# Optimization experiments

Measured on AMD Instinct MI355X. Metric: run time of the kernel, lower is better.

Reference implementation:

```python
import jax, jax.numpy as jnp
import numpy as np

N = 131072      # total nodes = num_graphs * numNodes
E = 2097152     # edges (avg degree 16)
C_IN = 64
HID = 64        # hiddenChannels
NODES = 128     # numNodes per graph
B = 1024        # num_graphs
NCLS = 4


def setup_inputs() -> dict:
    key = jax.random.key(0)
    ks = jax.random.split(key, 10)
    x = jax.random.normal(ks[0], (N, C_IN), jnp.float32)
    edge_index = jax.random.randint(ks[1], (2, E), 0, N, dtype=jnp.int32)
    edge_attr = jax.random.uniform(ks[2], (E,), jnp.float32)
    # GCNConv params (stored as [in, out]); PyG uses glorot init, bias zeros
    W1 = jax.random.normal(ks[3], (C_IN, 2 * HID), jnp.float32) * (1.0 / np.sqrt(C_IN))
    b1 = jnp.zeros((2 * HID,), jnp.float32)
    W2 = jax.random.normal(ks[4], (2 * HID, HID), jnp.float32) * (1.0 / np.sqrt(2 * HID))
    b2 = jnp.zeros((HID,), jnp.float32)
    Wfc = jax.random.normal(ks[5], (HID * NODES, NCLS), jnp.float32) * (1.0 / np.sqrt(HID * NODES))
    bfc = jnp.zeros((NCLS,), jnp.float32)
    return {"x": x, "edge_index": edge_index, "edge_attr": edge_attr,
            "W1": W1, "b1": b1, "W2": W2, "b2": b2, "Wfc": Wfc, "bfc": bfc}


def gcn_conv(x, src, dst, ew, W, b):
    # PyG GCNConv: add self-loops (weight 1), symmetric normalization,
    # linear transform, scatter-add aggregation at target nodes, + bias.
    loop = jnp.arange(N, dtype=src.dtype)
    s = jnp.concatenate([src, loop])
    d = jnp.concatenate([dst, loop])
    w = jnp.concatenate([ew, jnp.ones((N,), ew.dtype)])
    deg = jax.ops.segment_sum(w, d, num_segments=N)                  # [N]
    dis = jnp.where(deg > 0, jax.lax.rsqrt(jnp.maximum(deg, 1e-30)), 0.0)
    norm = dis[s] * w * dis[d]                                       # [E+N]
    h = x @ W                                                        # [N, out]
    msg = h[s] * norm[:, None]                                       # gather + scale
    out = jax.ops.segment_sum(msg, d, num_segments=N)                # scatter-add
    return out + b


def reference(x, edge_index, edge_attr, W1, b1, W2, b2, Wfc, bfc):
    src, dst = edge_index[0], edge_index[1]
    h = jax.nn.relu(gcn_conv(x, src, dst, edge_attr, W1, b1))
    h = jax.nn.relu(gcn_conv(h, src, dst, edge_attr, W2, b2))
    h = h.reshape(B, HID * NODES)
    logits = h @ Wfc + bfc
    return jax.nn.softmax(logits, axis=1)
```

## Files before the change

### kernel.cpp

```cpp
#include <hip/hip_runtime.h>

#define N_NODES 131072
#define NE      2097152
#define CIN     64
#define HID     64
#define H2X     128
#define NODESG  128
#define NGRAPH  1024
#define NCLS    4

#define NBUCK   256
#define NPB     512
#define HBLK    1024
#define EPB     2048
#define DEGSC   1048576.0f

typedef short bf16x8 __attribute__((ext_vector_type(8)));
typedef float f32x4  __attribute__((ext_vector_type(4)));

__device__ __forceinline__ unsigned short f2b(float f) {
    unsigned int u = __float_as_uint(f);
    return (unsigned short)((u + 0x7fffu + ((u >> 16) & 1u)) >> 16);
}
__device__ __forceinline__ unsigned int pack2(float a, float b) {
    return (unsigned int)f2b(a) | ((unsigned int)f2b(b) << 16);
}
__device__ __forceinline__ float blo(unsigned u) { return __uint_as_float(u << 16); }
__device__ __forceinline__ float bhi(unsigned u) { return __uint_as_float(u & 0xffff0000u); }


__global__ __launch_bounds__(256) void k_hist(const int* __restrict__ dst,
                                              int* __restrict__ hist) {
    __shared__ unsigned bh[NBUCK];
    int t = threadIdx.x;
    bh[t] = 0;
    __syncthreads();
    int base = blockIdx.x * EPB;
    #pragma unroll
    for (int k = 0; k < EPB / 256; ++k) {
        int d = dst[base + t + 256 * k];
        atomicAdd(&bh[d >> 9], 1u);
    }
    __syncthreads();
    hist[t * HBLK + blockIdx.x] = (int)bh[t];
}

__global__ void k_scan1(const int* __restrict__ in, int* __restrict__ out,
                        int* __restrict__ partial) {
    __shared__ int sd[256];
    int t = threadIdx.x;
    int base = blockIdx.x * 512;
    int c0 = in[base + 2*t];
    int c1 = in[base + 2*t + 1];
    int loc = c0 + c1;
    sd[t] = loc;
    __syncthreads();
    for (int off = 1; off < 256; off <<= 1) {
        int v = (t >= off) ? sd[t - off] : 0;
        __syncthreads();
        sd[t] += v;
        __syncthreads();
    }
    int excl = sd[t] - loc;
    out[base + 2*t]     = excl;
    out[base + 2*t + 1] = excl + c0;
    if (t == 255) partial[blockIdx.x] = sd[t];
}

__global__ void k_scan2(int* __restrict__ partial) {
    __shared__ int sd[256];
    int t = threadIdx.x;
    int p0 = partial[2*t], p1 = partial[2*t + 1];
    int loc = p0 + p1;
    sd[t] = loc;
    __syncthreads();
    for (int off = 1; off < 256; off <<= 1) {
        int v = (t >= off) ? sd[t - off] : 0;
        __syncthreads();
        sd[t] += v;
        __syncthreads();
    }
    int excl = sd[t] - loc;
    partial[2*t]     = excl;
    partial[2*t + 1] = excl + p0;
}

__global__ void k_scan3(int* __restrict__ data, const int* __restrict__ partial) {
    int i = blockIdx.x * blockDim.x + threadIdx.x;
    data[i] += partial[i >> 9];
}

__global__ __launch_bounds__(256) void k_scatter(
        const int* __restrict__ src, const int* __restrict__ dst,
        const float* __restrict__ ew, const int* __restrict__ hist,
        unsigned long long* __restrict__ part) {
    __shared__ unsigned lcur[NBUCK];
    int t = threadIdx.x;
    lcur[t] = (unsigned)hist[t * HBLK + blockIdx.x];
    __syncthreads();
    int base = blockIdx.x * EPB;
    #pragma unroll
    for (int k = 0; k < EPB / 256; ++k) {
        int e = base + t + 256 * k;
        int s = src[e], d = dst[e];
        unsigned w = __float_as_uint(ew[e]);
        unsigned p = atomicAdd(&lcur[d >> 9], 1u);
        part[p] = ((unsigned long long)w << 32) |
                  ((unsigned long long)(unsigned)(d & 511) << 17) |
                  (unsigned long long)(unsigned)s;
    }
}

__global__ __launch_bounds__(256) void k_bucket(
        const unsigned long long* __restrict__ part, const int* __restrict__ hist,
        int2* __restrict__ csr, int* __restrict__ rowptr,
        int* __restrict__ counts, float* __restrict__ dis) {
    __shared__ unsigned cnt[NPB];
    __shared__ unsigned degfx[NPB];
    __shared__ int rp[NPB];
    __shared__ int sd[256];
    int t = threadIdx.x, b = blockIdx.x;
    cnt[t] = 0; cnt[t + 256] = 0;
    degfx[t] = 0; degfx[t + 256] = 0;
    __syncthreads();
    int start = hist[b * HBLK];
    int end   = (b == NBUCK - 1) ? NE : hist[(b + 1) * HBLK];

    for (int j = start + t; j < end; j += 256) {
        unsigned long long p = part[j];
        unsigned dl = (unsigned)(p >> 17) & 511u;
        float w = __uint_as_float((unsigned)(p >> 32));
        atomicAdd(&cnt[dl], 1u);
        atomicAdd(&degfx[dl], (unsigned)(w * DEGSC));
    }
    __syncthreads();

    int c0 = (int)cnt[2*t], c1 = (int)cnt[2*t + 1];
    int loc = c0 + c1;
    sd[t] = loc;
    __syncthreads();
    for (int off = 1; off < 256; off <<= 1) {
        int v = (t >= off) ? sd[t - off] : 0;
        __syncthreads();
        sd[t] += v;
        __syncthreads();
    }
    int excl = sd[t] - loc;
    rp[2*t] = excl; rp[2*t + 1] = excl + c0;

    int n0 = b * NPB;
    rowptr[n0 + 2*t]     = start + excl;
    rowptr[n0 + 2*t + 1] = start + excl + c0;
    counts[n0 + 2*t]     = c0;
    counts[n0 + 2*t + 1] = c1;
    float dg0 = (float)degfx[2*t]     * (1.0f / DEGSC);
    float dg1 = (float)degfx[2*t + 1] * (1.0f / DEGSC);
    dis[n0 + 2*t]     = rsqrtf(dg0 + 1.0f);
    dis[n0 + 2*t + 1] = rsqrtf(dg1 + 1.0f);
    cnt[t] = 0; cnt[t + 256] = 0;
    __syncthreads();

    for (int j = start + t; j < end; j += 256) {
        unsigned long long p = part[j];
        unsigned dl = (unsigned)(p >> 17) & 511u;
        int s = (int)(p & 0x1ffffu);
        unsigned r = atomicAdd(&cnt[dl], 1u);
        csr[start + rp[dl] + (int)r] = make_int2(s, (int)(unsigned)(p >> 32));
    }
}

__global__ void k_xcast(const float* __restrict__ x, const float* __restrict__ dis,
                        uint2* __restrict__ xb2) {
    int i = blockIdx.x * blockDim.x + threadIdx.x;
    float d = dis[i >> 4];
    float4 v = ((const float4*)x)[i];
    xb2[i] = make_uint2(pack2(d * v.x, d * v.y), pack2(d * v.z, d * v.w));
}


#define GATHER_PAIR(TAB, pA, pB, nA, nB, cmA, cmB, a0,a1,a2,a3, b0,b1,b2,b3, vSA, vSB) \
    {                                                                                  \
        int   sA0 = __shfl(pA.x, qid),      sA1 = __shfl(pA.x, qid + 4);               \
        int   sA2 = __shfl(pA.x, qid + 8),  sA3 = __shfl(pA.x, qid + 12);              \
        float fA0 = __int_as_float(__shfl(pA.y, qid));                                 \
        float fA1 = __int_as_float(__shfl(pA.y, qid + 4));                             \
        float fA2 = __int_as_float(__shfl(pA.y, qid + 8));                             \
        float fA3 = __int_as_float(__shfl(pA.y, qid + 12));                            \
        int   sB0 = __shfl(pB.x, qid),      sB1 = __shfl(pB.x, qid + 4);               \
        int   sB2 = __shfl(pB.x, qid + 8),  sB3 = __shfl(pB.x, qid + 12);              \
        float fB0 = __int_as_float(__shfl(pB.y, qid));                                 \
        float fB1 = __int_as_float(__shfl(pB.y, qid + 4));                             \
        float fB2 = __int_as_float(__shfl(pB.y, qid + 8));                             \
        float fB3 = __int_as_float(__shfl(pB.y, qid + 12));                            \
        uint2 vA0 = TAB[((unsigned)sA0 << 4) | ql];                                    \
        uint2 vA1 = TAB[((unsigned)sA1 << 4) | ql];                                    \
        uint2 vA2 = TAB[((unsigned)sA2 << 4) | ql];                                    \
        uint2 vA3 = TAB[((unsigned)sA3 << 4) | ql];                                    \
        uint2 vB0 = TAB[((unsigned)sB0 << 4) | ql];                                    \
        uint2 vB1 = TAB[((unsigned)sB1 << 4) | ql];                                    \
        uint2 vB2 = TAB[((unsigned)sB2 << 4) | ql];                                    \
        uint2 vB3 = TAB[((unsigned)sB3 << 4) | ql];                                    \
        vSA = TAB[((unsigned)nA << 4) | ql];                                           \
        vSB = TAB[((unsigned)nB << 4) | ql];                                           \
        a0 = fmaf(fA0, blo(vA0.x), a0); a1 = fmaf(fA0, bhi(vA0.x), a1);                \
        a2 = fmaf(fA0, blo(vA0.y), a2); a3 = fmaf(fA0, bhi(vA0.y), a3);                \
        a0 = fmaf(fA1, blo(vA1.x), a0); a1 = fmaf(fA1, bhi(vA1.x), a1);                \
        a2 = fmaf(fA1, blo(vA1.y), a2); a3 = fmaf(fA1, bhi(vA1.y), a3);                \
        a0 = fmaf(fA2, blo(vA2.x), a0); a1 = fmaf(fA2, bhi(vA2.x), a1);                \
        a2 = fmaf(fA2, blo(vA2.y), a2); a3 = fmaf(fA2, bhi(vA2.y), a3);                \
        a0 = fmaf(fA3, blo(vA3.x), a0); a1 = fmaf(fA3, bhi(vA3.x), a1);                \
        a2 = fmaf(fA3, blo(vA3.y), a2); a3 = fmaf(fA3, bhi(vA3.y), a3);                \
        b0 = fmaf(fB0, blo(vB0.x), b0); b1 = fmaf(fB0, bhi(vB0.x), b1);                \
        b2 = fmaf(fB0, blo(vB0.y), b2); b3 = fmaf(fB0, bhi(vB0.y), b3);                \
        b0 = fmaf(fB1, blo(vB1.x), b0); b1 = fmaf(fB1, bhi(vB1.x), b1);                \
        b2 = fmaf(fB1, blo(vB1.y), b2); b3 = fmaf(fB1, bhi(vB1.y), b3);                \
        b0 = fmaf(fB2, blo(vB2.x), b0); b1 = fmaf(fB2, bhi(vB2.x), b1);                \
        b2 = fmaf(fB2, blo(vB2.y), b2); b3 = fmaf(fB2, bhi(vB2.y), b3);                \
        b0 = fmaf(fB3, blo(vB3.x), b0); b1 = fmaf(fB3, bhi(vB3.x), b1);                \
        b2 = fmaf(fB3, blo(vB3.y), b2); b3 = fmaf(fB3, bhi(vB3.y), b3);                \
        int tsA = (cmA > 16) ? ((cmA - 13) >> 2) : 0;                                  \
        for (int k = 0; k < tsA; ++k) {                                                \
            int jj = 16 + 4 * k + qid;                                                 \
            int   s = __shfl(pA.x, jj);                                                \
            float f = __int_as_float(__shfl(pA.y, jj));                                \
            uint2 v = TAB[((unsigned)s << 4) | ql];                                    \
            a0 = fmaf(f, blo(v.x), a0); a1 = fmaf(f, bhi(v.x), a1);                    \
            a2 = fmaf(f, blo(v.y), a2); a3 = fmaf(f, bhi(v.y), a3);                    \
        }                                                                              \
        int tsB = (cmB > 16) ? ((cmB - 13) >> 2) : 0;                                  \
        for (int k = 0; k < tsB; ++k) {                                                \
            int jj = 16 + 4 * k + qid;                                                 \
            int   s = __shfl(pB.x, jj);                                                \
            float f = __int_as_float(__shfl(pB.y, jj));                                \
            uint2 v = TAB[((unsigned)s << 4) | ql];                                    \
            b0 = fmaf(f, blo(v.x), b0); b1 = fmaf(f, bhi(v.x), b1);                    \
            b2 = fmaf(f, blo(v.y), b2); b3 = fmaf(f, bhi(v.y), b3);                    \
        }                                                                              \
        a0 += __shfl_xor(a0, 16); a1 += __shfl_xor(a1, 16);                            \
        a2 += __shfl_xor(a2, 16); a3 += __shfl_xor(a3, 16);                            \
        a0 += __shfl_xor(a0, 32); a1 += __shfl_xor(a1, 32);                            \
        a2 += __shfl_xor(a2, 32); a3 += __shfl_xor(a3, 32);                            \
        b0 += __shfl_xor(b0, 16); b1 += __shfl_xor(b1, 16);                            \
        b2 += __shfl_xor(b2, 16); b3 += __shfl_xor(b3, 16);                            \
        b0 += __shfl_xor(b0, 32); b1 += __shfl_xor(b1, 32);                            \
        b2 += __shfl_xor(b2, 32); b3 += __shfl_xor(b3, 32);                            \
    }


__global__ __launch_bounds__(256, 4) void k_layer1(
        const uint2* __restrict__ xb2, const int2* __restrict__ csr,
        const int* __restrict__ rowptr, const int* __restrict__ counts,
        const float* __restrict__ dis, const float* __restrict__ W1,
        const float* __restrict__ b1, unsigned short* __restrict__ h1b) {
    __shared__ unsigned short sWf[8192];
    __shared__ unsigned short sagg_b[32][72];
    __shared__ float sb[H2X];
    int tid = threadIdx.x;

    #pragma unroll
    for (int it = 0; it < 4; ++it) {
        int idx = tid + 256 * it;
        int kt = idx >> 9, nt = (idx >> 6) & 7, l = idx & 63;
        int lm = l & 15, lq = l >> 4;
        unsigned int pk[4];
        #pragma unroll
        for (int jp = 0; jp < 4; ++jp) {
            float w0 = W1[(kt*32 + lq*8 + 2*jp)     * H2X + nt*16 + lm];
            float w1 = W1[(kt*32 + lq*8 + 2*jp + 1) * H2X + nt*16 + lm];
            pk[jp] = pack2(w0, w1);
        }
        *(uint4*)&sWf[idx * 8] = make_uint4(pk[0], pk[1], pk[2], pk[3]);
    }
    if (tid < H2X) sb[tid] = b1[tid];

    int wave = tid >> 6, lane = tid & 63;
    int qid = lane >> 4, ql = lane & 15;
    int n0 = blockIdx.x * 32;
    int nb = n0 + wave * 8;

    int cm8[8], cnt8[8], rs8[8];
    float dn8[8];
    int2 myp[8];
    #pragma unroll
    for (int i = 0; i < 8; ++i) {
        rs8[i] = rowptr[nb + i];
        cnt8[i] = counts[nb + i];
        dn8[i] = dis[nb + i];
        cm8[i] = cnt8[i] < 64 ? cnt8[i] : 64;
    }
    #pragma unroll
    for (int i = 0; i < 8; ++i)
        myp[i] = (lane < cm8[i]) ? csr[rs8[i] + lane] : make_int2(0, 0);

    #pragma unroll
    for (int ip = 0; ip < 8; ip += 2) {
        int2 pA = myp[ip], pB = myp[ip + 1];
        int nA = nb + ip, nB = nA + 1;
        float a0 = 0.f, a1 = 0.f, a2 = 0.f, a3 = 0.f;
        float b0 = 0.f, b1v = 0.f, b2v = 0.f, b3 = 0.f;
        uint2 vSA, vSB;
        GATHER_PAIR(xb2, pA, pB, nA, nB, cm8[ip], cm8[ip + 1],
                    a0, a1, a2, a3, b0, b1v, b2v, b3, vSA, vSB);
        for (int jj = 64; jj < cnt8[ip]; ++jj) {
            int2 p = csr[rs8[ip] + jj];
            float f = __int_as_float(p.y);
            uint2 v = xb2[((unsigned)p.x << 4) | ql];
            if (qid == 0) {
                a0 += f * blo(v.x); a1 += f * bhi(v.x);
                a2 += f * blo(v.y); a3 += f * bhi(v.y);
            }
        }
        for (int jj = 64; jj < cnt8[ip + 1]; ++jj) {
            int2 p = csr[rs8[ip + 1] + jj];
            float f = __int_as_float(p.y);
            uint2 v = xb2[((unsigned)p.x << 4) | ql];
            if (qid == 0) {
                b0 += f * blo(v.x); b1v += f * bhi(v.x);
                b2v += f * blo(v.y); b3 += f * bhi(v.y);
            }
        }
        if (qid == 0) {
            float dnA = dn8[ip], dnB = dn8[ip + 1];
            int m = wave * 8 + ip;
            *(uint2*)&sagg_b[m][ql * 4] =
                make_uint2(pack2(dnA * (a0 + blo(vSA.x)), dnA * (a1 + bhi(vSA.x))),
                           pack2(dnA * (a2 + blo(vSA.y)), dnA * (a3 + bhi(vSA.y))));
            *(uint2*)&sagg_b[m + 1][ql * 4] =
                make_uint2(pack2(dnB * (b0 + blo(vSB.x)), dnB * (b1v + bhi(vSB.x))),
                           pack2(dnB * (b2v + blo(vSB.y)), dnB * (b3 + bhi(vSB.y))));
        }
    }
    __syncthreads();

    int mt = wave & 1, ntb = (wave >> 1) * 4;
    int lm = lane & 15, lq = lane >> 4;
    bf16x8 af0 = *(const bf16x8*)&sagg_b[mt*16 + lm][lq * 8];
    bf16x8 af1 = *(const bf16x8*)&sagg_b[mt*16 + lm][32 + lq * 8];
    #pragma unroll
    for (int t = 0; t < 4; ++t) {
        int nt = ntb + t;
        bf16x8 bf0 = *(const bf16x8*)&sWf[(nt*64 + lane) * 8];
        bf16x8 bf1 = *(const bf16x8*)&sWf[((8 + nt)*64 + lane) * 8];
        f32x4 acc = {0.f, 0.f, 0.f, 0.f};
        acc = __builtin_amdgcn_mfma_f32_16x16x32_bf16(af0, bf0, acc, 0, 0, 0);
        acc = __builtin_amdgcn_mfma_f32_16x16x32_bf16(af1, bf1, acc, 0, 0, 0);
        int ch = nt*16 + lm;
        float bias = sb[ch];
        #pragma unroll
        for (int r = 0; r < 4; ++r) {
            int node = n0 + mt*16 + lq*4 + r;
            h1b[(size_t)node * H2X + ch] = f2b(fmaxf(acc[r] + bias, 0.f));
        }
    }
}


__global__ __launch_bounds__(256) void k_gemm2(
        const unsigned short* __restrict__ h1b, const float* __restrict__ W2,
        const float* __restrict__ dis, unsigned short* __restrict__ t2u) {
    __shared__ unsigned short sWf[8192];
    __shared__ unsigned short sh[32][136];
    int tid = threadIdx.x;

    #pragma unroll
    for (int it = 0; it < 4; ++it) {
        int idx = tid + 256 * it;
        int kt = idx >> 8, nt = (idx >> 6) & 3, l = idx & 63;
        int lm = l & 15, lq = l >> 4;
        unsigned int pk[4];
        #pragma unroll
        for (int jp = 0; jp < 4; ++jp) {
            float w0 = W2[(kt*32 + lq*8 + 2*jp)     * HID + nt*16 + lm];
            float w1 = W2[(kt*32 + lq*8 + 2*jp + 1) * HID + nt*16 + lm];
            pk[jp] = pack2(w0, w1);
        }
        *(uint4*)&sWf[idx * 8] = make_uint4(pk[0], pk[1], pk[2], pk[3]);
    }

    int n0 = blockIdx.x * 32;
    #pragma unroll
    for (int it = 0; it < 2; ++it) {
        int idx = tid + 256 * it;
        int r = idx >> 4, c = idx & 15;
        *(uint4*)&sh[r][c * 8] = ((const uint4*)(h1b + (size_t)(n0 + r) * H2X))[c];
    }
    __syncthreads();

    int wave = tid >> 6, lane = tid & 63;
    int lm = lane & 15, lq = lane >> 4;
    #pragma unroll
    for (int ti = 0; ti < 2; ++ti) {
        int t = wave * 2 + ti;
        int mt = t & 1, nt = t >> 1;
        f32x4 acc = {0.f, 0.f, 0.f, 0.f};
        #pragma unroll
        for (int kt = 0; kt < 4; ++kt) {
            bf16x8 af = *(const bf16x8*)&sh[mt*16 + lm][kt*32 + lq*8];
            bf16x8 bf = *(const bf16x8*)&sWf[((kt*4 + nt)*64 + lane) * 8];
            acc = __builtin_amdgcn_mfma_f32_16x16x32_bf16(af, bf, acc, 0, 0, 0);
        }
        int ch = nt*16 + lm;
        #pragma unroll
        for (int r = 0; r < 4; ++r) {
            int node = n0 + mt*16 + lq*4 + r;
            t2u[(size_t)node * HID + ch] = f2b(dis[node] * acc[r]);
        }
    }
}


__global__ __launch_bounds__(256, 4) void k_agg2(
        const uint2* __restrict__ t2y, const int2* __restrict__ csr,
        const int* __restrict__ rowptr, const int* __restrict__ counts,
        const float* __restrict__ dis, const float* __restrict__ b2,
        unsigned short* __restrict__ h2b) {
    int tid = threadIdx.x;
    int wave = tid >> 6, lane = tid & 63;
    int qid = lane >> 4, ql = lane & 15;
    float4 bb = *(const float4*)&b2[ql * 4];
    int n0 = blockIdx.x * 32;
    int nb = n0 + wave * 8;

    int cm8[8], cnt8[8], rs8[8];
    float dn8[8];
    int2 myp[8];
    #pragma unroll
    for (int i = 0; i < 8; ++i) {
        rs8[i] = rowptr[nb + i];
        cnt8[i] = counts[nb + i];
        dn8[i] = dis[nb + i];
        cm8[i] = cnt8[i] < 64 ? cnt8[i] : 64;
    }
    #pragma unroll
    for (int i = 0; i < 8; ++i)
        myp[i] = (lane < cm8[i]) ? csr[rs8[i] + lane] : make_int2(0, 0);

    #pragma unroll
    for (int ip = 0; ip < 8; ip += 2) {
        int2 pA = myp[ip], pB = myp[ip + 1];
        int nA = nb + ip, nB = nA + 1;
        float a0 = 0.f, a1 = 0.f, a2 = 0.f, a3 = 0.f;
        float b0 = 0.f, b1v = 0.f, b2v = 0.f, b3 = 0.f;
        uint2 vSA, vSB;
        GATHER_PAIR(t2y, pA, pB, nA, nB, cm8[ip], cm8[ip + 1],
                    a0, a1, a2, a3, b0, b1v, b2v, b3, vSA, vSB);
        for (int jj = 64; jj < cnt8[ip]; ++jj) {
            int2 p = csr[rs8[ip] + jj];
            float f = __int_as_float(p.y);
            uint2 v = t2y[((unsigned)p.x << 4) | ql];
            if (qid == 0) {
                a0 += f * blo(v.x); a1 += f * bhi(v.x);
                a2 += f * blo(v.y); a3 += f * bhi(v.y);
            }
        }
        for (int jj = 64; jj < cnt8[ip + 1]; ++jj) {
            int2 p = csr[rs8[ip + 1] + jj];
            float f = __int_as_float(p.y);
            uint2 v = t2y[((unsigned)p.x << 4) | ql];
            if (qid == 0) {
                b0 += f * blo(v.x); b1v += f * bhi(v.x);
                b2v += f * blo(v.y); b3 += f * bhi(v.y);
            }
        }
        if (qid == 0) {
            float dnA = dn8[ip], dnB = dn8[ip + 1];
            float oa0 = fmaxf(fmaf(dnA, a0 + blo(vSA.x), bb.x), 0.f);
            float oa1 = fmaxf(fmaf(dnA, a1 + bhi(vSA.x), bb.y), 0.f);
            float oa2 = fmaxf(fmaf(dnA, a2 + blo(vSA.y), bb.z), 0.f);
            float oa3 = fmaxf(fmaf(dnA, a3 + bhi(vSA.y), bb.w), 0.f);
            float ob0 = fmaxf(fmaf(dnB, b0 + blo(vSB.x), bb.x), 0.f);
            float ob1 = fmaxf(fmaf(dnB, b1v + bhi(vSB.x), bb.y), 0.f);
            float ob2 = fmaxf(fmaf(dnB, b2v + blo(vSB.y), bb.z), 0.f);
            float ob3 = fmaxf(fmaf(dnB, b3 + bhi(vSB.y), bb.w), 0.f);
            *(uint2*)&h2b[((unsigned)nA << 6) | (ql * 4)] =
                make_uint2(pack2(oa0, oa1), pack2(oa2, oa3));
            *(uint2*)&h2b[((unsigned)nB << 6) | (ql * 4)] =
                make_uint2(pack2(ob0, ob1), pack2(ob2, ob3));
        }
    }
}


__global__ __launch_bounds__(256) void k_fc(
        const unsigned short* __restrict__ h2b, const float* __restrict__ Wfc,
        const float* __restrict__ bfc, float* __restrict__ out) {
    __shared__ float4 red[256];
    int b = blockIdx.x, t = threadIdx.x;
    const uint2* hrow = (const uint2*)(h2b + (size_t)b * (HID * NODESG));
    const float4* W4 = (const float4*)Wfc;
    float4 a = make_float4(0.f, 0.f, 0.f, 0.f);
    #pragma unroll
    for (int j = 0; j < 8; ++j) {
        int i = j * 256 + t;
        uint2 hv = hrow[i];
        float h0 = blo(hv.x), h1 = bhi(hv.x), h2v = blo(hv.y), h3 = bhi(hv.y);
        float4 w0 = W4[i * 4 + 0];
        float4 w1 = W4[i * 4 + 1];
        float4 w2 = W4[i * 4 + 2];
        float4 w3 = W4[i * 4 + 3];
        a.x = fmaf(h0, w0.x, a.x); a.y = fmaf(h0, w0.y, a.y);
        a.z = fmaf(h0, w0.z, a.z); a.w = fmaf(h0, w0.w, a.w);
        a.x = fmaf(h1, w1.x, a.x); a.y = fmaf(h1, w1.y, a.y);
        a.z = fmaf(h1, w1.z, a.z); a.w = fmaf(h1, w1.w, a.w);
        a.x = fmaf(h2v, w2.x, a.x); a.y = fmaf(h2v, w2.y, a.y);
        a.z = fmaf(h2v, w2.z, a.z); a.w = fmaf(h2v, w2.w, a.w);
        a.x = fmaf(h3, w3.x, a.x); a.y = fmaf(h3, w3.y, a.y);
        a.z = fmaf(h3, w3.z, a.z); a.w = fmaf(h3, w3.w, a.w);
    }
    red[t] = a;
    __syncthreads();
    for (int s = 128; s > 0; s >>= 1) {
        if (t < s) {
            red[t].x += red[t + s].x; red[t].y += red[t + s].y;
            red[t].z += red[t + s].z; red[t].w += red[t + s].w;
        }
        __syncthreads();
    }
    if (t == 0) {
        float l0 = red[0].x + bfc[0];
        float l1 = red[0].y + bfc[1];
        float l2 = red[0].z + bfc[2];
        float l3 = red[0].w + bfc[3];
        float mx = fmaxf(fmaxf(l0, l1), fmaxf(l2, l3));
        float e0 = expf(l0 - mx), e1 = expf(l1 - mx);
        float e2 = expf(l2 - mx), e3 = expf(l3 - mx);
        float inv = 1.f / (e0 + e1 + e2 + e3);
        float4 o = make_float4(e0 * inv, e1 * inv, e2 * inv, e3 * inv);
        *(float4*)&out[(size_t)b * 4] = o;
    }
}


extern "C" void kernel_launch(void* const* d_in, const int* in_sizes, int n_in,
                              void* d_out, int out_size, void* d_ws, size_t ws_size,
                              hipStream_t stream) {
    const float* x   = (const float*)d_in[0];
    const int*   ei  = (const int*)  d_in[1];
    const float* ea  = (const float*)d_in[2];
    const float* W1  = (const float*)d_in[3];
    const float* b1  = (const float*)d_in[4];
    const float* W2  = (const float*)d_in[5];
    const float* b2  = (const float*)d_in[6];
    const float* Wfc = (const float*)d_in[7];
    const float* bfc = (const float*)d_in[8];
    float* out = (float*)d_out;
    const int* src = ei;
    const int* dst = ei + NE;

    char* ws = (char*)d_ws;
    size_t off = 0;
    int*   hist   = (int*)  (ws + off); off += (size_t)NBUCK * HBLK * 4;
    int*   partial= (int*)  (ws + off); off += 4096;
    int*   counts = (int*)  (ws + off); off += (size_t)N_NODES * 4;
    int*   rowptr = (int*)  (ws + off); off += (size_t)N_NODES * 4;
    float* dis    = (float*)(ws + off); off += (size_t)N_NODES * 4;
    int2*  csr    = (int2*) (ws + off); off += (size_t)NE * 8;
    uint2* xb2    = (uint2*)(ws + off); off += (size_t)N_NODES * CIN * 2;
    unsigned short* h1b = (unsigned short*)(ws + off); off += (size_t)N_NODES * H2X * 2;
    unsigned short* t2u = (unsigned short*)(ws + off); off += (size_t)N_NODES * HID * 2;
    unsigned short* h2b = h1b;
    unsigned long long* part = (unsigned long long*)h1b;

    hipMemsetAsync(hist, 0, (size_t)NBUCK * HBLK * 4, stream);

    k_hist   <<<HBLK, 256, 0, stream>>>(dst, hist);
    k_scan1  <<<NBUCK * HBLK / 512, 256, 0, stream>>>(hist, hist, partial);
    k_scan2  <<<1, 256, 0, stream>>>(partial);
    k_scan3  <<<NBUCK * HBLK / 256, 256, 0, stream>>>(hist, partial);
    k_scatter<<<HBLK, 256, 0, stream>>>(src, dst, ea, hist, part);
    k_bucket <<<NBUCK, 256, 0, stream>>>(part, hist, csr, rowptr, counts, dis);
    k_xcast  <<<(N_NODES * CIN / 4) / 256, 256, 0, stream>>>(x, dis, xb2);
    k_layer1 <<<N_NODES / 32, 256, 0, stream>>>(xb2, csr, rowptr, counts, dis, W1, b1, h1b);
    k_gemm2  <<<N_NODES / 32, 256, 0, stream>>>(h1b, W2, dis, t2u);
    k_agg2   <<<N_NODES / 32, 256, 0, stream>>>((const uint2*)t2u, csr, rowptr, counts, dis, b2, h2b);
    k_fc     <<<NGRAPH, 256, 0, stream>>>(h2b, Wfc, bfc, out);
}
```

Before: 278.4 us.

## Fuse layer-2 GEMM into layer-1 kernel and pre-swizzle weights once

Layer 1 now writes its ReLU output to shared memory and immediately runs the layer-2 GEMM there, removing the k_gemm2 launch and the round trip of the 128-wide h1 activation through global memory. Weight packing into MFMA fragment layout moves to a single-block prologue kernel, so blocks read pre-swizzled bf16 weights from global/L2 instead of each block repacking them into LDS. In k_bucket, the edge count and the fixed-point degree are packed into one 64-bit LDS atomic, halving the atomics in the first pass. The costs are extra LDS for the h1 tile, B fragments now loaded from global memory, and a tiny extra launch.

```diff
diff --git a/kernel.cpp b/kernel.cpp
--- a/kernel.cpp
+++ b/kernel.cpp
@@ -14,6 +14,7 @@
 #define HBLK    1024
 #define EPB     2048
 #define DEGSC   1048576.0f
+#define DEGMASK ((1ull << 40) - 1)
 
 typedef short bf16x8 __attribute__((ext_vector_type(8)));
 typedef float f32x4  __attribute__((ext_vector_type(4)));
@@ -27,6 +28,41 @@
 }
 __device__ __forceinline__ float blo(unsigned u) { return __uint_as_float(u << 16); }
 __device__ __forceinline__ float bhi(unsigned u) { return __uint_as_float(u & 0xffff0000u); }
+
+
+__global__ __launch_bounds__(256) void k_wswiz(
+        const float* __restrict__ W1, const float* __restrict__ W2,
+        unsigned short* __restrict__ wf1, unsigned short* __restrict__ wf2) {
+    int tid = threadIdx.x;
+    #pragma unroll
+    for (int it = 0; it < 4; ++it) {
+        int idx = tid + 256 * it;
+        int kt = idx >> 9, nt = (idx >> 6) & 7, l = idx & 63;
+        int lm = l & 15, lq = l >> 4;
+        unsigned pk[4];
+        #pragma unroll
+        for (int jp = 0; jp < 4; ++jp) {
+            float w0 = W1[(kt*32 + lq*8 + 2*jp)     * H2X + nt*16 + lm];
+            float w1 = W1[(kt*32 + lq*8 + 2*jp + 1) * H2X + nt*16 + lm];
+            pk[jp] = pack2(w0, w1);
+        }
+        *(uint4*)&wf1[idx * 8] = make_uint4(pk[0], pk[1], pk[2], pk[3]);
+    }
+    #pragma unroll
+    for (int it = 0; it < 4; ++it) {
+        int idx = tid + 256 * it;
+        int kt = idx >> 8, nt = (idx >> 6) & 3, l = idx & 63;
+        int lm = l & 15, lq = l >> 4;
+        unsigned pk[4];
+        #pragma unroll
+        for (int jp = 0; jp < 4; ++jp) {
+            float w0 = W2[(kt*32 + lq*8 + 2*jp)     * HID + nt*16 + lm];
+            float w1 = W2[(kt*32 + lq*8 + 2*jp + 1) * HID + nt*16 + lm];
+            pk[jp] = pack2(w0, w1);
+        }
+        *(uint4*)&wf2[idx * 8] = make_uint4(pk[0], pk[1], pk[2], pk[3]);
+    }
+}
 
 
 __global__ __launch_bounds__(256) void k_hist(const int* __restrict__ dst,
@@ -115,13 +151,13 @@
         const unsigned long long* __restrict__ part, const int* __restrict__ hist,
         int2* __restrict__ csr, int* __restrict__ rowptr,
         int* __restrict__ counts, float* __restrict__ dis) {
-    __shared__ unsigned cnt[NPB];
-    __shared__ unsigned degfx[NPB];
+    __shared__ unsigned long long dc[NPB];
+    __shared__ unsigned cnt2[NPB];
     __shared__ int rp[NPB];
     __shared__ int sd[256];
     int t = threadIdx.x, b = blockIdx.x;
-    cnt[t] = 0; cnt[t + 256] = 0;
-    degfx[t] = 0; degfx[t + 256] = 0;
+    dc[t] = 0; dc[t + 256] = 0;
+    cnt2[t] = 0; cnt2[t + 256] = 0;
     __syncthreads();
     int start = hist[b * HBLK];
     int end   = (b == NBUCK - 1) ? NE : hist[(b + 1) * HBLK];
@@ -130,12 +166,12 @@
         unsigned long long p = part[j];
         unsigned dl = (unsigned)(p >> 17) & 511u;
         float w = __uint_as_float((unsigned)(p >> 32));
-        atomicAdd(&cnt[dl], 1u);
-        atomicAdd(&degfx[dl], (unsigned)(w * DEGSC));
-    }
-    __syncthreads();
-
-    int c0 = (int)cnt[2*t], c1 = (int)cnt[2*t + 1];
+        atomicAdd(&dc[dl], (1ull << 40) | (unsigned long long)(unsigned)(w * DEGSC));
+    }
+    __syncthreads();
+
+    unsigned long long d0 = dc[2*t], d1 = dc[2*t + 1];
+    int c0 = (int)(d0 >> 40), c1 = (int)(d1 >> 40);
     int loc = c0 + c1;
     sd[t] = loc;
     __syncthreads();
@@ -153,18 +189,17 @@
     rowptr[n0 + 2*t + 1] = start + excl + c0;
     counts[n0 + 2*t]     = c0;
     counts[n0 + 2*t + 1] = c1;
-    float dg0 = (float)degfx[2*t]     * (1.0f / DEGSC);
-    float dg1 = (float)degfx[2*t + 1] * (1.0f / DEGSC);
+    float dg0 = (float)(d0 & DEGMASK) * (1.0f / DEGSC);
+    float dg1 = (float)(d1 & DEGMASK) * (1.0f / DEGSC);
     dis[n0 + 2*t]     = rsqrtf(dg0 + 1.0f);
     dis[n0 + 2*t + 1] = rsqrtf(dg1 + 1.0f);
-    cnt[t] = 0; cnt[t + 256] = 0;
     __syncthreads();
 
     for (int j = start + t; j < end; j += 256) {
         unsigned long long p = part[j];
         unsigned dl = (unsigned)(p >> 17) & 511u;
         int s = (int)(p & 0x1ffffu);
-        unsigned r = atomicAdd(&cnt[dl], 1u);
+        unsigned r = atomicAdd(&cnt2[dl], 1u);
         csr[start + rp[dl] + (int)r] = make_int2(s, (int)(unsigned)(p >> 32));
     }
 }
@@ -250,27 +285,13 @@
 __global__ __launch_bounds__(256, 4) void k_layer1(
         const uint2* __restrict__ xb2, const int2* __restrict__ csr,
         const int* __restrict__ rowptr, const int* __restrict__ counts,
-        const float* __restrict__ dis, const float* __restrict__ W1,
-        const float* __restrict__ b1, unsigned short* __restrict__ h1b) {
-    __shared__ unsigned short sWf[8192];
+        const float* __restrict__ dis, const unsigned short* __restrict__ wf1,
+        const unsigned short* __restrict__ wf2, const float* __restrict__ b1,
+        unsigned short* __restrict__ t2u) {
     __shared__ unsigned short sagg_b[32][72];
+    __shared__ unsigned short sh1[32][136];
     __shared__ float sb[H2X];
     int tid = threadIdx.x;
-
-    #pragma unroll
-    for (int it = 0; it < 4; ++it) {
-        int idx = tid + 256 * it;
-        int kt = idx >> 9, nt = (idx >> 6) & 7, l = idx & 63;
-        int lm = l & 15, lq = l >> 4;
-        unsigned int pk[4];
-        #pragma unroll
-        for (int jp = 0; jp < 4; ++jp) {
-            float w0 = W1[(kt*32 + lq*8 + 2*jp)     * H2X + nt*16 + lm];
-            float w1 = W1[(kt*32 + lq*8 + 2*jp + 1) * H2X + nt*16 + lm];
-            pk[jp] = pack2(w0, w1);
-        }
-        *(uint4*)&sWf[idx * 8] = make_uint4(pk[0], pk[1], pk[2], pk[3]);
-    }
     if (tid < H2X) sb[tid] = b1[tid];
 
     int wave = tid >> 6, lane = tid & 63;
@@ -339,70 +360,34 @@
     #pragma unroll
     for (int t = 0; t < 4; ++t) {
         int nt = ntb + t;
-        bf16x8 bf0 = *(const bf16x8*)&sWf[(nt*64 + lane) * 8];
-        bf16x8 bf1 = *(const bf16x8*)&sWf[((8 + nt)*64 + lane) * 8];
+        bf16x8 bf0 = *(const bf16x8*)&wf1[(nt*64 + lane) * 8];
+        bf16x8 bf1 = *(const bf16x8*)&wf1[((8 + nt)*64 + lane) * 8];
         f32x4 acc = {0.f, 0.f, 0.f, 0.f};
         acc = __builtin_amdgcn_mfma_f32_16x16x32_bf16(af0, bf0, acc, 0, 0, 0);
         acc = __builtin_amdgcn_mfma_f32_16x16x32_bf16(af1, bf1, acc, 0, 0, 0);
         int ch = nt*16 + lm;
         float bias = sb[ch];
         #pragma unroll
-        for (int r = 0; r < 4; ++r) {
-            int node = n0 + mt*16 + lq*4 + r;
-            h1b[(size_t)node * H2X + ch] = f2b(fmaxf(acc[r] + bias, 0.f));
-        }
-    }
-}
-
-
-__global__ __launch_bounds__(256) void k_gemm2(
-        const unsigned short* __restrict__ h1b, const float* __restrict__ W2,
-        const float* __restrict__ dis, unsigned short* __restrict__ t2u) {
-    __shared__ unsigned short sWf[8192];
-    __shared__ unsigned short sh[32][136];
-    int tid = threadIdx.x;
-
-    #pragma unroll
-    for (int it = 0; it < 4; ++it) {
-        int idx = tid + 256 * it;
-        int kt = idx >> 8, nt = (idx >> 6) & 3, l = idx & 63;
-        int lm = l & 15, lq = l >> 4;
-        unsigned int pk[4];
-        #pragma unroll
-        for (int jp = 0; jp < 4; ++jp) {
-            float w0 = W2[(kt*32 + lq*8 + 2*jp)     * HID + nt*16 + lm];
-            float w1 = W2[(kt*32 + lq*8 + 2*jp + 1) * HID + nt*16 + lm];
-            pk[jp] = pack2(w0, w1);
-        }
-        *(uint4*)&sWf[idx * 8] = make_uint4(pk[0], pk[1], pk[2], pk[3]);
-    }
-
-    int n0 = blockIdx.x * 32;
-    #pragma unroll
-    for (int it = 0; it < 2; ++it) {
-        int idx = tid + 256 * it;
-        int r = idx >> 4, c = idx & 15;
-        *(uint4*)&sh[r][c * 8] = ((const uint4*)(h1b + (size_t)(n0 + r) * H2X))[c];
-    }
-    __syncthreads();
-
-    int wave = tid >> 6, lane = tid & 63;
-    int lm = lane & 15, lq = lane >> 4;
+        for (int r = 0; r < 4; ++r)
+            sh1[mt*16 + lq*4 + r][ch] = f2b(fmaxf(acc[r] + bias, 0.f));
+    }
+    __syncthreads();
+
     #pragma unroll
     for (int ti = 0; ti < 2; ++ti) {
         int t = wave * 2 + ti;
-        int mt = t & 1, nt = t >> 1;
+        int mt2 = t & 1, nt2 = t >> 1;
         f32x4 acc = {0.f, 0.f, 0.f, 0.f};
         #pragma unroll
         for (int kt = 0; kt < 4; ++kt) {
-            bf16x8 af = *(const bf16x8*)&sh[mt*16 + lm][kt*32 + lq*8];
-            bf16x8 bf = *(const bf16x8*)&sWf[((kt*4 + nt)*64 + lane) * 8];
+            bf16x8 af = *(const bf16x8*)&sh1[mt2*16 + lm][kt*32 + lq*8];
+            bf16x8 bf = *(const bf16x8*)&wf2[((kt*4 + nt2)*64 + lane) * 8];
             acc = __builtin_amdgcn_mfma_f32_16x16x32_bf16(af, bf, acc, 0, 0, 0);
         }
-        int ch = nt*16 + lm;
+        int ch = nt2*16 + lm;
         #pragma unroll
         for (int r = 0; r < 4; ++r) {
-            int node = n0 + mt*16 + lq*4 + r;
+            int node = n0 + mt2*16 + lq*4 + r;
             t2u[(size_t)node * HID + ch] = f2b(dis[node] * acc[r]);
         }
     }
@@ -554,15 +539,17 @@
     int*   counts = (int*)  (ws + off); off += (size_t)N_NODES * 4;
     int*   rowptr = (int*)  (ws + off); off += (size_t)N_NODES * 4;
     float* dis    = (float*)(ws + off); off += (size_t)N_NODES * 4;
+    unsigned short* wf1 = (unsigned short*)(ws + off); off += 8192 * 2;
+    unsigned short* wf2 = (unsigned short*)(ws + off); off += 8192 * 2;
     int2*  csr    = (int2*) (ws + off); off += (size_t)NE * 8;
     uint2* xb2    = (uint2*)(ws + off); off += (size_t)N_NODES * CIN * 2;
-    unsigned short* h1b = (unsigned short*)(ws + off); off += (size_t)N_NODES * H2X * 2;
     unsigned short* t2u = (unsigned short*)(ws + off); off += (size_t)N_NODES * HID * 2;
-    unsigned short* h2b = h1b;
-    unsigned long long* part = (unsigned long long*)h1b;
+    unsigned short* h2b = (unsigned short*)(ws + off); off += (size_t)N_NODES * HID * 2;
+    unsigned long long* part = (unsigned long long*)h2b;
 
     hipMemsetAsync(hist, 0, (size_t)NBUCK * HBLK * 4, stream);
 
+    k_wswiz  <<<1, 256, 0, stream>>>(W1, W2, wf1, wf2);
     k_hist   <<<HBLK, 256, 0, stream>>>(dst, hist);
     k_scan1  <<<NBUCK * HBLK / 512, 256, 0, stream>>>(hist, hist, partial);
     k_scan2  <<<1, 256, 0, stream>>>(partial);
@@ -570,8 +557,9 @@
     k_scatter<<<HBLK, 256, 0, stream>>>(src, dst, ea, hist, part);
     k_bucket <<<NBUCK, 256, 0, stream>>>(part, hist, csr, rowptr, counts, dis);
     k_xcast  <<<(N_NODES * CIN / 4) / 256, 256, 0, stream>>>(x, dis, xb2);
-    k_layer1 <<<N_NODES / 32, 256, 0, stream>>>(xb2, csr, rowptr, counts, dis, W1, b1, h1b);
-    k_gemm2  <<<N_NODES / 32, 256, 0, stream>>>(h1b, W2, dis, t2u);
-    k_agg2   <<<N_NODES / 32, 256, 0, stream>>>((const uint2*)t2u, csr, rowptr, counts, dis, b2, h2b);
+    k_layer1 <<<N_NODES / 32, 256, 0, stream>>>(xb2, csr, rowptr, counts, dis,
+                                                wf1, wf2, b1, t2u);
+    k_agg2   <<<N_NODES / 32, 256, 0, stream>>>((const uint2*)t2u, csr, rowptr,
+                                                counts, dis, b2, h2b);
     k_fc     <<<NGRAPH, 256, 0, stream>>>(h2b, Wfc, bfc, out);
 }
```

After: 271.0 us. 1.03x faster.
